# Kernel optimization log

Hardware: AMD Instinct MI355X
Metric: run time of the kernel (lower is better)

Reference implementation:

```python
import jax, jax.numpy as jnp
import numpy as np

N_NODES = 100000
N_EDGES = 1600000
MAX_RADIUS = 3.0
NUM_BASIS = 3
SQRT2 = 2.0 ** 0.5
# e3nn soft_one_hot_linspace 'smooth_finite' prefactor
C_SMOOTH = 1.14136 * float(np.exp(2.0))


def _sus(x):
    # smooth unit step: exp(-1/x) for x>0 else 0 (NaN-safe for grad)
    safe = jnp.where(x > 0.0, x, 1.0)
    return jnp.where(x > 0.0, jnp.exp(-1.0 / safe), 0.0)


def radial_embed(d):
    # soft_one_hot_linspace(d, 0, max_radius, 3, basis='smooth_finite', cutoff=True) * sqrt(num_basis)
    values = jnp.linspace(0.0, MAX_RADIUS, NUM_BASIS + 2)[1:-1]  # [3]
    step = MAX_RADIUS / (NUM_BASIS + 1)
    diff = (d[:, None] - values) / step  # [E,3]
    y = C_SMOOTH * _sus(diff + 1.0) * _sus(1.0 - diff)
    return y * (NUM_BASIS ** 0.5)


def fcnet(x, w1, w2):
    # e3nn FullyConnectedNet([3,16,numel], relu): normalized weights, normalize2mom(relu)=sqrt(2)*relu
    h = SQRT2 * jax.nn.relu(x @ (w1 / w1.shape[0] ** 0.5))
    return h @ (w2 / w2.shape[0] ** 0.5)


def reference(pos, feat, edge_src, edge_dst, fc1_w1, fc1_w2, core_w1, core_w2, fc3_w1, fc3_w2, conv_w, conv_b):
    n = pos.shape[0]
    z = edge_src.shape[0] / n  # average num neighbors
    edge_vec = pos[edge_dst] - pos[edge_src]
    d = jnp.sqrt(jnp.sum(edge_vec * edge_vec, axis=1))  # edges are self-loop-free -> d > 0
    emb = radial_embed(d)  # [E,3]

    # NOTE on e3nn math: with input/mid/output parities all even and sh = 0e+1o+2e,
    # the only parity-allowed paths producing nonzero output are the 0e (scalar) paths,
    # which contract against Y_0 = 1 ('component' normalization). The 4x1e block of the
    # mid irreps is identically zero (no parity-allowed path ever populates it), so the
    # math below (scalar block only, with e3nn path weights) is exactly equivalent.
    def conv(x, w1, w2, mul_in, mul_out, path_w):
        # per-edge weights from radial MLP; keep the 0e->0e instruction block
        w = fcnet(emb, w1, w2)[:, : mul_in * mul_out].reshape(-1, mul_in, mul_out)
        msg = path_w * jnp.einsum('euw,eu->ew', w, x[edge_src])
        return jax.ops.segment_sum(msg, edge_dst, num_segments=n) / z ** 0.5

    x = conv(feat, fc1_w1, fc1_w2, 3, 4, (1.0 / 3.0) ** 0.5)  # tp1: fan_in 3*1 -> pw=1/sqrt(3)
    for i in range(3):
        x = conv(x, core_w1[i], core_w2[i], 4, 4, 0.5)  # tp2 0e path: pw=sqrt(1/4)
    x = conv(x, fc3_w1, fc3_w2, 4, 16, 0.5)  # tp3: pw=sqrt(1/4)
    # Conv1d(16, 2, 1) == pointwise linear
    return x @ conv_w.T + conv_b


def setup_inputs():
    key = jax.random.key(0)
    ks = jax.random.split(key, 12)
    pos = jax.random.uniform(ks[0], (N_NODES, 3), dtype=jnp.float32)  # unit box -> all edge lengths < max_radius
    feat = jax.random.normal(ks[1], (N_NODES, 3), dtype=jnp.float32)
    edge_src = jax.random.randint(ks[2], (N_EDGES,), 0, N_NODES, dtype=jnp.int32)
    off = jax.random.randint(ks[3], (N_EDGES,), 1, N_NODES, dtype=jnp.int32)
    edge_dst = ((edge_src + off) % N_NODES).astype(jnp.int32)  # radius_graph has no self-loops
    return {
        'pos': pos,
        'feat': feat,
        'edge_src': edge_src,
        'edge_dst': edge_dst,
        'fc1_w1': jax.random.normal(ks[4], (3, 16), jnp.float32),
        'fc1_w2': jax.random.normal(ks[5], (16, 12), jnp.float32),
        'core_w1': jax.random.normal(ks[6], (3, 3, 16), jnp.float32),
        'core_w2': jax.random.normal(ks[7], (3, 16, 48), jnp.float32),
        'fc3_w1': jax.random.normal(ks[8], (3, 16), jnp.float32),
        'fc3_w2': jax.random.normal(ks[9], (16, 64), jnp.float32),
        'conv_w': jax.random.normal(ks[10], (2, 16), jnp.float32) * 0.25,
        'conv_b': jax.random.normal(ks[11], (2,), jnp.float32) * 0.1,
    }
```

## Files before the change

### kernel.cpp

```cpp
#include <hip/hip_runtime.h>


#define BCAP 4608
#define NBMAX 400

__device__ __forceinline__ float sus_f(float x) {
    return x > 0.0f ? __expf(-1.0f / x) : 0.0f;
}

__device__ __forceinline__ float uload(const float* p) {
    return __uint_as_float(__builtin_amdgcn_readfirstlane(__float_as_uint(*p)));
}

__global__ __launch_bounds__(256) void k_bin(
    const int* __restrict__ src, const int* __restrict__ dst,
    int* __restrict__ gcur, int* __restrict__ ptmp,
    const float* __restrict__ fc3w2, const float* __restrict__ cw,
    float* __restrict__ gbuf,
    int nedges, int nb)
{
    __shared__ int cnt[NBMAX];
    __shared__ int gb[NBMAX];
    for (int b = threadIdx.x; b < nb; b += 256) cnt[b] = 0;
    __syncthreads();

    int base = blockIdx.x * 2048 + threadIdx.x * 8;
    int pk[8]; int bk[8]; short r[8];
    int ss[8], dd[8];
    if (base + 7 < nedges) {
        int4 s0 = *(const int4*)&src[base];
        int4 s1 = *(const int4*)&src[base + 4];
        int4 d0 = *(const int4*)&dst[base];
        int4 d1 = *(const int4*)&dst[base + 4];
        ss[0]=s0.x; ss[1]=s0.y; ss[2]=s0.z; ss[3]=s0.w;
        ss[4]=s1.x; ss[5]=s1.y; ss[6]=s1.z; ss[7]=s1.w;
        dd[0]=d0.x; dd[1]=d0.y; dd[2]=d0.z; dd[3]=d0.w;
        dd[4]=d1.x; dd[5]=d1.y; dd[6]=d1.z; dd[7]=d1.w;
        #pragma unroll
        for (int i = 0; i < 8; ++i) {
            int b = dd[i] >> 8;
            bk[i] = b;
            pk[i] = (ss[i] << 8) | (dd[i] & 255);
            r[i] = (short)atomicAdd(&cnt[b], 1);
        }
    } else {
        #pragma unroll
        for (int i = 0; i < 8; ++i) {
            int e = base + i;
            if (e < nedges) {
                int s = src[e], t = dst[e];
                int b = t >> 8;
                bk[i] = b;
                pk[i] = (s << 8) | (t & 255);
                r[i] = (short)atomicAdd(&cnt[b], 1);
            } else bk[i] = -1;
        }
    }
    __syncthreads();
    for (int b = threadIdx.x; b < nb; b += 256) {
        int c = cnt[b];
        gb[b] = c > 0 ? atomicAdd(&gcur[b], c) : 0;
    }
    __syncthreads();
    #pragma unroll
    for (int i = 0; i < 8; ++i) {
        if (bk[i] >= 0) {
            int p = gb[bk[i]] + (int)r[i];
            if (p < BCAP)
                ptmp[bk[i] * BCAP + p] = pk[i];
        }
    }

    if (blockIdx.x == 0 && threadIdx.x < 128) {
        int idx = threadIdx.x;
        int k = idx >> 3, u = (idx >> 1) & 3, c = idx & 1;
        float s = 0.0f;
        #pragma unroll
        for (int w = 0; w < 16; ++w)
            s = fmaf(fc3w2[k * 64 + u * 16 + w], cw[c * 16 + w], s);
        gbuf[idx] = s;
    }
}

__global__ __launch_bounds__(256) void k_build(
    const int* __restrict__ gcur, const int* __restrict__ ptmp,
    int* __restrict__ pidx, int2* __restrict__ offs2,
    int n, int nb)
{
    int b = blockIdx.x;
    int cnt = gcur[b]; if (cnt > BCAP) cnt = BCAP;

    __shared__ int stage[BCAP];
    __shared__ int perm[BCAP];
    __shared__ int deg[256];
    __shared__ int loffs[256];
    __shared__ int cur[256];

    const int* tin = ptmp + b * BCAP;
    for (int j = threadIdx.x; j < cnt; j += 256) stage[j] = tin[j];
    deg[threadIdx.x] = 0;
    __syncthreads();

    for (int j = threadIdx.x; j < cnt; j += 256)
        atomicAdd(&deg[stage[j] & 255], 1);
    __syncthreads();

    {
        int t = threadIdx.x;
        int v = deg[t];
        loffs[t] = v; __syncthreads();
        for (int off = 1; off < 256; off <<= 1) {
            int val = (t >= off) ? loffs[t - off] : 0;
            __syncthreads();
            loffs[t] += val;
            __syncthreads();
        }
        int incl = loffs[t];
        __syncthreads();
        loffs[t] = incl - v;
        cur[t] = incl - v;
        __syncthreads();
    }

    {
        int nid0 = b << 8;
        int nn = n - nid0; if (nn > 256) nn = 256;
        int t = threadIdx.x;
        if (t < nn) {
            int st = b * BCAP + loffs[t];
            offs2[nid0 + t] = make_int2(st, st + deg[t]);
        }
    }

    for (int j = threadIdx.x; j < cnt; j += 256) {
        int pkd = stage[j];
        perm[atomicAdd(&cur[pkd & 255], 1)] = pkd;
    }
    __syncthreads();

    int* tout = pidx + b * BCAP;
    for (int j = threadIdx.x; j < cnt; j += 256) tout[j] = perm[j];
}

__global__ __launch_bounds__(256) void k_emb(
    const float* __restrict__ pos, const int* __restrict__ gcur,
    const int* __restrict__ pidx, float4* __restrict__ ebuf)
{
    int b = blockIdx.y;
    int j = blockIdx.x * 256 + threadIdx.x;
    if (j >= gcur[b]) return;
    int pkd = pidx[b * BCAP + j];
    int s = pkd >> 8;
    int t = (b << 8) | (pkd & 255);
    float dx = pos[3 * t + 0] - pos[3 * s + 0];
    float dy = pos[3 * t + 1] - pos[3 * s + 1];
    float dz = pos[3 * t + 2] - pos[3 * s + 2];
    float d = sqrtf(dx * dx + dy * dy + dz * dz);
    const float C = 1.14136f * 7.3890560989306495f;
    float e0, e1, e2;
    { float f = (d - 0.75f) * (1.0f / 0.75f);
      e0 = C * sus_f(f + 1.0f) * sus_f(1.0f - f); }
    { float f = (d - 1.50f) * (1.0f / 0.75f);
      e1 = C * sus_f(f + 1.0f) * sus_f(1.0f - f); }
    { float f = (d - 2.25f) * (1.0f / 0.75f);
      e2 = C * sus_f(f + 1.0f) * sus_f(1.0f - f); }
    ebuf[(size_t)b * BCAP + j] = make_float4(__int_as_float(s), e0, e1, e2);
}


__global__ __launch_bounds__(256) void k_node_l1(
    const float* __restrict__ feat, const float4* __restrict__ edata,
    const int2* __restrict__ offs2,
    const float* __restrict__ w1, const float* __restrict__ w2,
    float* __restrict__ xout, int n)
{
    __shared__ float lw[16 * 20];
    if (threadIdx.x < 192) {
        int k = threadIdx.x / 12, r = threadIdx.x % 12;
        lw[k * 20 + r] = w2[k * 12 + r];
    }
    __syncthreads();

    int g = blockIdx.x * 256 + threadIdx.x;
    int nd = g >> 2;
    if (nd >= n) return;
    int t = g & 3;

    float w1r[3][16];
    #pragma unroll
    for (int j = 0; j < 3; ++j)
        #pragma unroll
        for (int k = 0; k < 16; ++k) w1r[j][k] = uload(&w1[j * 16 + k]);

    float O[16][3];
    #pragma unroll
    for (int k = 0; k < 16; ++k)
        #pragma unroll
        for (int u = 0; u < 3; ++u) O[k][u] = 0.0f;

    int2 se = offs2[nd];
    for (int e = se.x + t; e < se.y; e += 4) {
        float4 ed = edata[e];
        int s = __float_as_int(ed.x);
        float f0 = feat[3 * s + 0], f1 = feat[3 * s + 1], f2 = feat[3 * s + 2];
        #pragma unroll
        for (int k = 0; k < 16; ++k) {
            float a = fmaf(ed.y, w1r[0][k], fmaf(ed.z, w1r[1][k], ed.w * w1r[2][k]));
            float h = a > 0.0f ? a : 0.0f;
            O[k][0] = fmaf(h, f0, O[k][0]);
            O[k][1] = fmaf(h, f1, O[k][1]);
            O[k][2] = fmaf(h, f2, O[k][2]);
        }
    }

    float p0 = 0.f, p1 = 0.f, p2 = 0.f, p3 = 0.f;
    #pragma unroll
    for (int k = 0; k < 16; ++k)
        #pragma unroll
        for (int u = 0; u < 3; ++u) {
            const float4 q = *(const float4*)&lw[k * 20 + u * 4];
            float o = O[k][u];
            p0 = fmaf(o, q.x, p0); p1 = fmaf(o, q.y, p1);
            p2 = fmaf(o, q.z, p2); p3 = fmaf(o, q.w, p3);
        }
    p0 += __shfl_xor(p0, 1); p1 += __shfl_xor(p1, 1);
    p2 += __shfl_xor(p2, 1); p3 += __shfl_xor(p3, 1);
    p0 += __shfl_xor(p0, 2); p1 += __shfl_xor(p1, 2);
    p2 += __shfl_xor(p2, 2); p3 += __shfl_xor(p3, 2);
    if (t == 0) {
        const float S = 0.051031036307982884f;
        float4 o; o.x = p0 * S; o.y = p1 * S; o.z = p2 * S; o.w = p3 * S;
        ((float4*)xout)[nd] = o;
    }
}

__global__ __launch_bounds__(256) void k_node_core(
    const float4* __restrict__ xin, const float4* __restrict__ edata,
    const int2* __restrict__ offs2,
    const float* __restrict__ w1, const float* __restrict__ w2,
    float* __restrict__ xout, int n)
{
    __shared__ float lw[16 * 20];
    {
        int idx = threadIdx.x;
        int k = idx >> 4, r = idx & 15;
        lw[k * 20 + r] = w2[k * 48 + r];
    }
    __syncthreads();

    int g = blockIdx.x * 256 + threadIdx.x;
    int nd = g >> 2;
    if (nd >= n) return;
    int t = g & 3;

    float w1r[3][16];
    #pragma unroll
    for (int j = 0; j < 3; ++j)
        #pragma unroll
        for (int k = 0; k < 16; ++k) w1r[j][k] = uload(&w1[j * 16 + k]);

    float O[16][4];
    #pragma unroll
    for (int k = 0; k < 16; ++k)
        #pragma unroll
        for (int u = 0; u < 4; ++u) O[k][u] = 0.0f;

    int2 se = offs2[nd];
    for (int e = se.x + t; e < se.y; e += 4) {
        float4 ed = edata[e];
        int s = __float_as_int(ed.x);
        float4 x = xin[s];
        #pragma unroll
        for (int k = 0; k < 16; ++k) {
            float a = fmaf(ed.y, w1r[0][k], fmaf(ed.z, w1r[1][k], ed.w * w1r[2][k]));
            float h = a > 0.0f ? a : 0.0f;
            O[k][0] = fmaf(h, x.x, O[k][0]);
            O[k][1] = fmaf(h, x.y, O[k][1]);
            O[k][2] = fmaf(h, x.z, O[k][2]);
            O[k][3] = fmaf(h, x.w, O[k][3]);
        }
    }

    float p0 = 0.f, p1 = 0.f, p2 = 0.f, p3 = 0.f;
    #pragma unroll
    for (int k = 0; k < 16; ++k)
        #pragma unroll
        for (int u = 0; u < 4; ++u) {
            const float4 q = *(const float4*)&lw[k * 20 + u * 4];
            float o = O[k][u];
            p0 = fmaf(o, q.x, p0); p1 = fmaf(o, q.y, p1);
            p2 = fmaf(o, q.z, p2); p3 = fmaf(o, q.w, p3);
        }
    p0 += __shfl_xor(p0, 1); p1 += __shfl_xor(p1, 1);
    p2 += __shfl_xor(p2, 1); p3 += __shfl_xor(p3, 1);
    p0 += __shfl_xor(p0, 2); p1 += __shfl_xor(p1, 2);
    p2 += __shfl_xor(p2, 2); p3 += __shfl_xor(p3, 2);
    if (t == 0) {
        const float S = 0.04419417382415922f;
        float4 o; o.x = p0 * S; o.y = p1 * S; o.z = p2 * S; o.w = p3 * S;
        ((float4*)xout)[nd] = o;
    }
}

__global__ __launch_bounds__(256) void k_node_fc3_final(
    const float4* __restrict__ xin, const float4* __restrict__ edata,
    const int2* __restrict__ offs2,
    const float* __restrict__ w1, const float* __restrict__ gbuf,
    const float* __restrict__ cb,
    float* __restrict__ out, int n)
{
    __shared__ float lg[128];
    if (threadIdx.x < 128) lg[threadIdx.x] = gbuf[threadIdx.x];
    __syncthreads();

    int g = blockIdx.x * 256 + threadIdx.x;
    int nd = g >> 2;
    if (nd >= n) return;
    int t = g & 3;

    float w1r[3][16];
    #pragma unroll
    for (int j = 0; j < 3; ++j)
        #pragma unroll
        for (int k = 0; k < 16; ++k) w1r[j][k] = uload(&w1[j * 16 + k]);

    float O[16][4];
    #pragma unroll
    for (int k = 0; k < 16; ++k)
        #pragma unroll
        for (int u = 0; u < 4; ++u) O[k][u] = 0.0f;

    int2 se = offs2[nd];
    for (int e = se.x + t; e < se.y; e += 4) {
        float4 ed = edata[e];
        int s = __float_as_int(ed.x);
        float4 x = xin[s];
        #pragma unroll
        for (int k = 0; k < 16; ++k) {
            float a = fmaf(ed.y, w1r[0][k], fmaf(ed.z, w1r[1][k], ed.w * w1r[2][k]));
            float h = a > 0.0f ? a : 0.0f;
            O[k][0] = fmaf(h, x.x, O[k][0]);
            O[k][1] = fmaf(h, x.y, O[k][1]);
            O[k][2] = fmaf(h, x.z, O[k][2]);
            O[k][3] = fmaf(h, x.w, O[k][3]);
        }
    }

    float a0 = 0.f, a1 = 0.f;
    #pragma unroll
    for (int k = 0; k < 16; ++k)
        #pragma unroll
        for (int u = 0; u < 4; ++u) {
            float o = O[k][u];
            const float2 q = *(const float2*)&lg[(k * 4 + u) * 2];
            a0 = fmaf(o, q.x, a0);
            a1 = fmaf(o, q.y, a1);
        }
    a0 += __shfl_xor(a0, 1); a1 += __shfl_xor(a1, 1);
    a0 += __shfl_xor(a0, 2); a1 += __shfl_xor(a1, 2);
    if (t == 0) {
        const float S = 0.04419417382415922f;
        float2 o; o.x = fmaf(a0, S, cb[0]); o.y = fmaf(a1, S, cb[1]);
        ((float2*)out)[nd] = o;
    }
}


extern "C" void kernel_launch(void* const* d_in, const int* in_sizes, int n_in,
                              void* d_out, int out_size, void* d_ws, size_t ws_size,
                              hipStream_t stream) {
    const float* pos     = (const float*)d_in[0];
    const float* feat    = (const float*)d_in[1];
    const int*   esrc    = (const int*)d_in[2];
    const int*   edst    = (const int*)d_in[3];
    const float* fc1_w1  = (const float*)d_in[4];
    const float* fc1_w2  = (const float*)d_in[5];
    const float* core_w1 = (const float*)d_in[6];
    const float* core_w2 = (const float*)d_in[7];
    const float* fc3_w1  = (const float*)d_in[8];
    const float* fc3_w2  = (const float*)d_in[9];
    const float* conv_w  = (const float*)d_in[10];
    const float* conv_b  = (const float*)d_in[11];
    float* out = (float*)d_out;

    const int E = in_sizes[2];
    const int N = in_sizes[0] / 3;
    const int nb = (N + 255) >> 8;

    float4* ebuf = (float4*)d_ws;
    int* ptmp  = (int*)(ebuf + (size_t)nb * BCAP);
    int* pidx  = ptmp + (size_t)nb * BCAP;
    float* xa  = (float*)(pidx + (size_t)nb * BCAP);
    float* xb  = xa + (size_t)4 * N;
    int2* offs2 = (int2*)(xb + (size_t)4 * N);
    int* gcur  = (int*)(offs2 + N);
    float* gbuf = (float*)(gcur + ((nb + 3) & ~3));

    int g4 = (4 * N + 255) / 256;

    hipMemsetAsync(gcur, 0, (size_t)nb * sizeof(int), stream);
    k_bin<<<(E + 2047) / 2048, 256, 0, stream>>>(esrc, edst, gcur, ptmp,
                                                 fc3_w2, conv_w, gbuf, E, nb);
    k_build<<<nb, 256, 0, stream>>>(gcur, ptmp, pidx, offs2, N, nb);
    {
        dim3 eg(BCAP / 256, nb);
        k_emb<<<eg, 256, 0, stream>>>(pos, gcur, pidx, ebuf);
    }

    k_node_l1<<<g4, 256, 0, stream>>>(feat, ebuf, offs2, fc1_w1, fc1_w2, xa, N);
    k_node_core<<<g4, 256, 0, stream>>>((const float4*)xa, ebuf, offs2,
                                        core_w1 + 0, core_w2 + 0, xb, N);
    k_node_core<<<g4, 256, 0, stream>>>((const float4*)xb, ebuf, offs2,
                                        core_w1 + 48, core_w2 + 768, xa, N);
    k_node_core<<<g4, 256, 0, stream>>>((const float4*)xa, ebuf, offs2,
                                        core_w1 + 96, core_w2 + 1536, xb, N);
    k_node_fc3_final<<<g4, 256, 0, stream>>>((const float4*)xb, ebuf, offs2,
                                             fc3_w1, gbuf, conv_b, out, N);
}
```

Measured before the change: 236.6 us.

## Fuse five node-layer kernels into one cooperative persistent kernel with grid syncs

Replaces the five per-layer node kernels with a single cooperative kernel. It loops over tiles persistently and places grid.sync between layers, sized from occupancy times 256 CUs. This removes four kernel launches and their tail and drain gaps. In exchange it adds grid-wide barrier costs, and __launch_bounds__(256,4) may cap registers or occupancy for the unrolled 64-accumulator loops.

```diff
diff --git a/kernel.cpp b/kernel.cpp
--- a/kernel.cpp
+++ b/kernel.cpp
@@ -1,4 +1,7 @@
 #include <hip/hip_runtime.h>
+#include <hip/hip_cooperative_groups.h>
+
+namespace cg = cooperative_groups;
 
 
 #define BCAP 4608
@@ -167,201 +170,206 @@
     ebuf[(size_t)b * BCAP + j] = make_float4(__int_as_float(s), e0, e1, e2);
 }
 
-
-__global__ __launch_bounds__(256) void k_node_l1(
+__global__ __launch_bounds__(256, 4) void k_layers(
     const float* __restrict__ feat, const float4* __restrict__ edata,
     const int2* __restrict__ offs2,
-    const float* __restrict__ w1, const float* __restrict__ w2,
-    float* __restrict__ xout, int n)
+    const float* __restrict__ fc1w1, const float* __restrict__ fc1w2,
+    const float* __restrict__ corew1, const float* __restrict__ corew2,
+    const float* __restrict__ fc3w1, const float* __restrict__ gbuf,
+    const float* __restrict__ cb,
+    float* __restrict__ xa, float* __restrict__ xb,
+    float* __restrict__ out, int n)
 {
     __shared__ float lw[16 * 20];
+    cg::grid_group grid = cg::this_grid();
+    const int items = 4 * n;
+    const int ntiles = (items + 255) >> 8;
+    const int t = threadIdx.x & 3;
+
     if (threadIdx.x < 192) {
         int k = threadIdx.x / 12, r = threadIdx.x % 12;
-        lw[k * 20 + r] = w2[k * 12 + r];
-    }
-    __syncthreads();
-
-    int g = blockIdx.x * 256 + threadIdx.x;
-    int nd = g >> 2;
-    if (nd >= n) return;
-    int t = g & 3;
-
-    float w1r[3][16];
-    #pragma unroll
-    for (int j = 0; j < 3; ++j)
-        #pragma unroll
-        for (int k = 0; k < 16; ++k) w1r[j][k] = uload(&w1[j * 16 + k]);
-
-    float O[16][3];
-    #pragma unroll
-    for (int k = 0; k < 16; ++k)
-        #pragma unroll
-        for (int u = 0; u < 3; ++u) O[k][u] = 0.0f;
-
-    int2 se = offs2[nd];
-    for (int e = se.x + t; e < se.y; e += 4) {
-        float4 ed = edata[e];
-        int s = __float_as_int(ed.x);
-        float f0 = feat[3 * s + 0], f1 = feat[3 * s + 1], f2 = feat[3 * s + 2];
-        #pragma unroll
-        for (int k = 0; k < 16; ++k) {
-            float a = fmaf(ed.y, w1r[0][k], fmaf(ed.z, w1r[1][k], ed.w * w1r[2][k]));
-            float h = a > 0.0f ? a : 0.0f;
-            O[k][0] = fmaf(h, f0, O[k][0]);
-            O[k][1] = fmaf(h, f1, O[k][1]);
-            O[k][2] = fmaf(h, f2, O[k][2]);
-        }
-    }
-
-    float p0 = 0.f, p1 = 0.f, p2 = 0.f, p3 = 0.f;
-    #pragma unroll
-    for (int k = 0; k < 16; ++k)
-        #pragma unroll
-        for (int u = 0; u < 3; ++u) {
-            const float4 q = *(const float4*)&lw[k * 20 + u * 4];
-            float o = O[k][u];
-            p0 = fmaf(o, q.x, p0); p1 = fmaf(o, q.y, p1);
-            p2 = fmaf(o, q.z, p2); p3 = fmaf(o, q.w, p3);
-        }
-    p0 += __shfl_xor(p0, 1); p1 += __shfl_xor(p1, 1);
-    p2 += __shfl_xor(p2, 1); p3 += __shfl_xor(p3, 1);
-    p0 += __shfl_xor(p0, 2); p1 += __shfl_xor(p1, 2);
-    p2 += __shfl_xor(p2, 2); p3 += __shfl_xor(p3, 2);
-    if (t == 0) {
-        const float S = 0.051031036307982884f;
-        float4 o; o.x = p0 * S; o.y = p1 * S; o.z = p2 * S; o.w = p3 * S;
-        ((float4*)xout)[nd] = o;
-    }
-}
-
-__global__ __launch_bounds__(256) void k_node_core(
-    const float4* __restrict__ xin, const float4* __restrict__ edata,
-    const int2* __restrict__ offs2,
-    const float* __restrict__ w1, const float* __restrict__ w2,
-    float* __restrict__ xout, int n)
-{
-    __shared__ float lw[16 * 20];
-    {
-        int idx = threadIdx.x;
-        int k = idx >> 4, r = idx & 15;
-        lw[k * 20 + r] = w2[k * 48 + r];
-    }
-    __syncthreads();
-
-    int g = blockIdx.x * 256 + threadIdx.x;
-    int nd = g >> 2;
-    if (nd >= n) return;
-    int t = g & 3;
-
-    float w1r[3][16];
-    #pragma unroll
-    for (int j = 0; j < 3; ++j)
-        #pragma unroll
-        for (int k = 0; k < 16; ++k) w1r[j][k] = uload(&w1[j * 16 + k]);
-
-    float O[16][4];
-    #pragma unroll
-    for (int k = 0; k < 16; ++k)
-        #pragma unroll
-        for (int u = 0; u < 4; ++u) O[k][u] = 0.0f;
-
-    int2 se = offs2[nd];
-    for (int e = se.x + t; e < se.y; e += 4) {
-        float4 ed = edata[e];
-        int s = __float_as_int(ed.x);
-        float4 x = xin[s];
-        #pragma unroll
-        for (int k = 0; k < 16; ++k) {
-            float a = fmaf(ed.y, w1r[0][k], fmaf(ed.z, w1r[1][k], ed.w * w1r[2][k]));
-            float h = a > 0.0f ? a : 0.0f;
-            O[k][0] = fmaf(h, x.x, O[k][0]);
-            O[k][1] = fmaf(h, x.y, O[k][1]);
-            O[k][2] = fmaf(h, x.z, O[k][2]);
-            O[k][3] = fmaf(h, x.w, O[k][3]);
-        }
-    }
-
-    float p0 = 0.f, p1 = 0.f, p2 = 0.f, p3 = 0.f;
-    #pragma unroll
-    for (int k = 0; k < 16; ++k)
-        #pragma unroll
-        for (int u = 0; u < 4; ++u) {
-            const float4 q = *(const float4*)&lw[k * 20 + u * 4];
-            float o = O[k][u];
-            p0 = fmaf(o, q.x, p0); p1 = fmaf(o, q.y, p1);
-            p2 = fmaf(o, q.z, p2); p3 = fmaf(o, q.w, p3);
-        }
-    p0 += __shfl_xor(p0, 1); p1 += __shfl_xor(p1, 1);
-    p2 += __shfl_xor(p2, 1); p3 += __shfl_xor(p3, 1);
-    p0 += __shfl_xor(p0, 2); p1 += __shfl_xor(p1, 2);
-    p2 += __shfl_xor(p2, 2); p3 += __shfl_xor(p3, 2);
-    if (t == 0) {
-        const float S = 0.04419417382415922f;
-        float4 o; o.x = p0 * S; o.y = p1 * S; o.z = p2 * S; o.w = p3 * S;
-        ((float4*)xout)[nd] = o;
-    }
-}
-
-__global__ __launch_bounds__(256) void k_node_fc3_final(
-    const float4* __restrict__ xin, const float4* __restrict__ edata,
-    const int2* __restrict__ offs2,
-    const float* __restrict__ w1, const float* __restrict__ gbuf,
-    const float* __restrict__ cb,
-    float* __restrict__ out, int n)
-{
-    __shared__ float lg[128];
-    if (threadIdx.x < 128) lg[threadIdx.x] = gbuf[threadIdx.x];
-    __syncthreads();
-
-    int g = blockIdx.x * 256 + threadIdx.x;
-    int nd = g >> 2;
-    if (nd >= n) return;
-    int t = g & 3;
-
-    float w1r[3][16];
-    #pragma unroll
-    for (int j = 0; j < 3; ++j)
-        #pragma unroll
-        for (int k = 0; k < 16; ++k) w1r[j][k] = uload(&w1[j * 16 + k]);
-
-    float O[16][4];
-    #pragma unroll
-    for (int k = 0; k < 16; ++k)
-        #pragma unroll
-        for (int u = 0; u < 4; ++u) O[k][u] = 0.0f;
-
-    int2 se = offs2[nd];
-    for (int e = se.x + t; e < se.y; e += 4) {
-        float4 ed = edata[e];
-        int s = __float_as_int(ed.x);
-        float4 x = xin[s];
-        #pragma unroll
-        for (int k = 0; k < 16; ++k) {
-            float a = fmaf(ed.y, w1r[0][k], fmaf(ed.z, w1r[1][k], ed.w * w1r[2][k]));
-            float h = a > 0.0f ? a : 0.0f;
-            O[k][0] = fmaf(h, x.x, O[k][0]);
-            O[k][1] = fmaf(h, x.y, O[k][1]);
-            O[k][2] = fmaf(h, x.z, O[k][2]);
-            O[k][3] = fmaf(h, x.w, O[k][3]);
-        }
-    }
-
-    float a0 = 0.f, a1 = 0.f;
-    #pragma unroll
-    for (int k = 0; k < 16; ++k)
-        #pragma unroll
-        for (int u = 0; u < 4; ++u) {
-            float o = O[k][u];
-            const float2 q = *(const float2*)&lg[(k * 4 + u) * 2];
-            a0 = fmaf(o, q.x, a0);
-            a1 = fmaf(o, q.y, a1);
-        }
-    a0 += __shfl_xor(a0, 1); a1 += __shfl_xor(a1, 1);
-    a0 += __shfl_xor(a0, 2); a1 += __shfl_xor(a1, 2);
-    if (t == 0) {
-        const float S = 0.04419417382415922f;
-        float2 o; o.x = fmaf(a0, S, cb[0]); o.y = fmaf(a1, S, cb[1]);
-        ((float2*)out)[nd] = o;
+        lw[k * 20 + r] = fc1w2[k * 12 + r];
+    }
+    __syncthreads();
+    {
+        float w1r[3][16];
+        #pragma unroll
+        for (int j = 0; j < 3; ++j)
+            #pragma unroll
+            for (int k = 0; k < 16; ++k) w1r[j][k] = uload(&fc1w1[j * 16 + k]);
+
+        for (int tile = blockIdx.x; tile < ntiles; tile += gridDim.x) {
+            int it = (tile << 8) + threadIdx.x;
+            if (it >= items) continue;
+            int nd = it >> 2;
+
+            float O[16][3];
+            #pragma unroll
+            for (int k = 0; k < 16; ++k)
+                #pragma unroll
+                for (int u = 0; u < 3; ++u) O[k][u] = 0.0f;
+
+            int2 se = offs2[nd];
+            for (int e = se.x + t; e < se.y; e += 4) {
+                float4 ed = edata[e];
+                int s = __float_as_int(ed.x);
+                float f0 = feat[3 * s + 0], f1 = feat[3 * s + 1], f2 = feat[3 * s + 2];
+                #pragma unroll
+                for (int k = 0; k < 16; ++k) {
+                    float a = fmaf(ed.y, w1r[0][k], fmaf(ed.z, w1r[1][k], ed.w * w1r[2][k]));
+                    float h = a > 0.0f ? a : 0.0f;
+                    O[k][0] = fmaf(h, f0, O[k][0]);
+                    O[k][1] = fmaf(h, f1, O[k][1]);
+                    O[k][2] = fmaf(h, f2, O[k][2]);
+                }
+            }
+
+            float p0 = 0.f, p1 = 0.f, p2 = 0.f, p3 = 0.f;
+            #pragma unroll
+            for (int k = 0; k < 16; ++k)
+                #pragma unroll
+                for (int u = 0; u < 3; ++u) {
+                    const float4 q = *(const float4*)&lw[k * 20 + u * 4];
+                    float o = O[k][u];
+                    p0 = fmaf(o, q.x, p0); p1 = fmaf(o, q.y, p1);
+                    p2 = fmaf(o, q.z, p2); p3 = fmaf(o, q.w, p3);
+                }
+            p0 += __shfl_xor(p0, 1); p1 += __shfl_xor(p1, 1);
+            p2 += __shfl_xor(p2, 1); p3 += __shfl_xor(p3, 1);
+            p0 += __shfl_xor(p0, 2); p1 += __shfl_xor(p1, 2);
+            p2 += __shfl_xor(p2, 2); p3 += __shfl_xor(p3, 2);
+            if (t == 0) {
+                const float S = 0.051031036307982884f;
+                float4 o; o.x = p0 * S; o.y = p1 * S; o.z = p2 * S; o.w = p3 * S;
+                ((float4*)xa)[nd] = o;
+            }
+        }
+    }
+    grid.sync();
+
+    for (int c = 0; c < 3; ++c) {
+        const float*  w1p  = corew1 + 48 * c;
+        const float*  w2p  = corew2 + 768 * c;
+        const float4* xin  = (const float4*)((c == 1) ? xb : xa);
+        float*        xout = (c == 1) ? xa : xb;
+
+        {
+            int k = threadIdx.x >> 4, r = threadIdx.x & 15;
+            lw[k * 20 + r] = w2p[k * 48 + r];
+        }
+        __syncthreads();
+
+        float w1r[3][16];
+        #pragma unroll
+        for (int j = 0; j < 3; ++j)
+            #pragma unroll
+            for (int k = 0; k < 16; ++k) w1r[j][k] = uload(&w1p[j * 16 + k]);
+
+        for (int tile = blockIdx.x; tile < ntiles; tile += gridDim.x) {
+            int it = (tile << 8) + threadIdx.x;
+            if (it >= items) continue;
+            int nd = it >> 2;
+
+            float O[16][4];
+            #pragma unroll
+            for (int k = 0; k < 16; ++k)
+                #pragma unroll
+                for (int u = 0; u < 4; ++u) O[k][u] = 0.0f;
+
+            int2 se = offs2[nd];
+            for (int e = se.x + t; e < se.y; e += 4) {
+                float4 ed = edata[e];
+                int s = __float_as_int(ed.x);
+                float4 x = xin[s];
+                #pragma unroll
+                for (int k = 0; k < 16; ++k) {
+                    float a = fmaf(ed.y, w1r[0][k], fmaf(ed.z, w1r[1][k], ed.w * w1r[2][k]));
+                    float h = a > 0.0f ? a : 0.0f;
+                    O[k][0] = fmaf(h, x.x, O[k][0]);
+                    O[k][1] = fmaf(h, x.y, O[k][1]);
+                    O[k][2] = fmaf(h, x.z, O[k][2]);
+                    O[k][3] = fmaf(h, x.w, O[k][3]);
+                }
+            }
+
+            float p0 = 0.f, p1 = 0.f, p2 = 0.f, p3 = 0.f;
+            #pragma unroll
+            for (int k = 0; k < 16; ++k)
+                #pragma unroll
+                for (int u = 0; u < 4; ++u) {
+                    const float4 q = *(const float4*)&lw[k * 20 + u * 4];
+                    float o = O[k][u];
+                    p0 = fmaf(o, q.x, p0); p1 = fmaf(o, q.y, p1);
+                    p2 = fmaf(o, q.z, p2); p3 = fmaf(o, q.w, p3);
+                }
+            p0 += __shfl_xor(p0, 1); p1 += __shfl_xor(p1, 1);
+            p2 += __shfl_xor(p2, 1); p3 += __shfl_xor(p3, 1);
+            p0 += __shfl_xor(p0, 2); p1 += __shfl_xor(p1, 2);
+            p2 += __shfl_xor(p2, 2); p3 += __shfl_xor(p3, 2);
+            if (t == 0) {
+                const float S = 0.04419417382415922f;
+                float4 o; o.x = p0 * S; o.y = p1 * S; o.z = p2 * S; o.w = p3 * S;
+                ((float4*)xout)[nd] = o;
+            }
+        }
+        grid.sync();
+    }
+
+    if (threadIdx.x < 128) lw[threadIdx.x] = gbuf[threadIdx.x];
+    __syncthreads();
+    {
+        const float4* xin = (const float4*)xb;
+        float w1r[3][16];
+        #pragma unroll
+        for (int j = 0; j < 3; ++j)
+            #pragma unroll
+            for (int k = 0; k < 16; ++k) w1r[j][k] = uload(&fc3w1[j * 16 + k]);
+
+        for (int tile = blockIdx.x; tile < ntiles; tile += gridDim.x) {
+            int it = (tile << 8) + threadIdx.x;
+            if (it >= items) continue;
+            int nd = it >> 2;
+
+            float O[16][4];
+            #pragma unroll
+            for (int k = 0; k < 16; ++k)
+                #pragma unroll
+                for (int u = 0; u < 4; ++u) O[k][u] = 0.0f;
+
+            int2 se = offs2[nd];
+            for (int e = se.x + t; e < se.y; e += 4) {
+                float4 ed = edata[e];
+                int s = __float_as_int(ed.x);
+                float4 x = xin[s];
+                #pragma unroll
+                for (int k = 0; k < 16; ++k) {
+                    float a = fmaf(ed.y, w1r[0][k], fmaf(ed.z, w1r[1][k], ed.w * w1r[2][k]));
+                    float h = a > 0.0f ? a : 0.0f;
+                    O[k][0] = fmaf(h, x.x, O[k][0]);
+                    O[k][1] = fmaf(h, x.y, O[k][1]);
+                    O[k][2] = fmaf(h, x.z, O[k][2]);
+                    O[k][3] = fmaf(h, x.w, O[k][3]);
+                }
+            }
+
+            float a0 = 0.f, a1 = 0.f;
+            #pragma unroll
+            for (int k = 0; k < 16; ++k)
+                #pragma unroll
+                for (int u = 0; u < 4; ++u) {
+                    float o = O[k][u];
+                    const float2 q = *(const float2*)&lw[(k * 4 + u) * 2];
+                    a0 = fmaf(o, q.x, a0);
+                    a1 = fmaf(o, q.y, a1);
+                }
+            a0 += __shfl_xor(a0, 1); a1 += __shfl_xor(a1, 1);
+            a0 += __shfl_xor(a0, 2); a1 += __shfl_xor(a1, 2);
+            if (t == 0) {
+                const float S = 0.04419417382415922f;
+                float2 o; o.x = fmaf(a0, S, cb[0]); o.y = fmaf(a1, S, cb[1]);
+                ((float2*)out)[nd] = o;
+            }
+        }
     }
 }
 
@@ -396,8 +404,6 @@
     int* gcur  = (int*)(offs2 + N);
     float* gbuf = (float*)(gcur + ((nb + 3) & ~3));
 
-    int g4 = (4 * N + 255) / 256;
-
     hipMemsetAsync(gcur, 0, (size_t)nb * sizeof(int), stream);
     k_bin<<<(E + 2047) / 2048, 256, 0, stream>>>(esrc, edst, gcur, ptmp,
                                                  fc3_w2, conv_w, gbuf, E, nb);
@@ -407,13 +413,23 @@
         k_emb<<<eg, 256, 0, stream>>>(pos, gcur, pidx, ebuf);
     }
 
-    k_node_l1<<<g4, 256, 0, stream>>>(feat, ebuf, offs2, fc1_w1, fc1_w2, xa, N);
-    k_node_core<<<g4, 256, 0, stream>>>((const float4*)xa, ebuf, offs2,
-                                        core_w1 + 0, core_w2 + 0, xb, N);
-    k_node_core<<<g4, 256, 0, stream>>>((const float4*)xb, ebuf, offs2,
-                                        core_w1 + 48, core_w2 + 768, xa, N);
-    k_node_core<<<g4, 256, 0, stream>>>((const float4*)xa, ebuf, offs2,
-                                        core_w1 + 96, core_w2 + 1536, xb, N);
-    k_node_fc3_final<<<g4, 256, 0, stream>>>((const float4*)xb, ebuf, offs2,
-                                             fc3_w1, gbuf, conv_b, out, N);
-}
+    {
+        int nbpc = 0;
+        hipOccupancyMaxActiveBlocksPerMultiprocessor(
+            &nbpc, reinterpret_cast<const void*>(k_layers), 256, 0);
+        if (nbpc < 1) nbpc = 1;
+        int ntiles = (4 * N + 255) / 256;
+        int gsize = nbpc * 256;
+        if (gsize > ntiles) gsize = ntiles;
+
+        void* kargs[] = {
+            (void*)&feat, (void*)&ebuf, (void*)&offs2,
+            (void*)&fc1_w1, (void*)&fc1_w2,
+            (void*)&core_w1, (void*)&core_w2,
+            (void*)&fc3_w1, (void*)&gbuf, (void*)&conv_b,
+            (void*)&xa, (void*)&xb, (void*)&out, (void*)&N
+        };
+        hipLaunchCooperativeKernel(reinterpret_cast<const void*>(k_layers),
+                                   dim3(gsize), dim3(256), kargs, 0, stream);
+    }
+}
```

Result: slower. 859.0 us (+263.0%).

## Balance edge work per block with contiguous chunks and LDS atomic accumulation

Applied to the files above, without the earlier changes.

Replaces the four-threads-per-node split with a scheme where each 128-node block divides its contiguous CSR edge range evenly across 256 threads. Each thread accumulates the partial 16x4 hidden-feature sums for runs of edges that share a destination node, then flushes them into a per-node shared-memory accumulator with LDS atomics. The per-node output projection is done afterwards from shared memory. The goal is to remove load imbalance caused by varying node degrees. The cost is LDS atomics at run boundaries, a large shared-memory footprint that limits occupancy, and the edge buffer now storing the packed index so each thread can find the destination.

```diff
diff --git a/kernel.cpp b/kernel.cpp
--- a/kernel.cpp
+++ b/kernel.cpp
@@ -3,6 +3,7 @@
 
 #define BCAP 4608
 #define NBMAX 400
+#define OSTR 68
 
 __device__ __forceinline__ float sus_f(float x) {
     return x > 0.0f ? __expf(-1.0f / x) : 0.0f;
@@ -164,27 +165,34 @@
       e1 = C * sus_f(f + 1.0f) * sus_f(1.0f - f); }
     { float f = (d - 2.25f) * (1.0f / 0.75f);
       e2 = C * sus_f(f + 1.0f) * sus_f(1.0f - f); }
-    ebuf[(size_t)b * BCAP + j] = make_float4(__int_as_float(s), e0, e1, e2);
-}
-
-
-__global__ __launch_bounds__(256) void k_node_l1(
+    ebuf[(size_t)b * BCAP + j] = make_float4(__int_as_float(pkd), e0, e1, e2);
+}
+
+
+__global__ __launch_bounds__(256) void k_layer_l1(
     const float* __restrict__ feat, const float4* __restrict__ edata,
     const int2* __restrict__ offs2,
     const float* __restrict__ w1, const float* __restrict__ w2,
     float* __restrict__ xout, int n)
 {
+    __shared__ float Oacc[128 * OSTR];
     __shared__ float lw[16 * 20];
     if (threadIdx.x < 192) {
         int k = threadIdx.x / 12, r = threadIdx.x % 12;
         lw[k * 20 + r] = w2[k * 12 + r];
     }
-    __syncthreads();
-
-    int g = blockIdx.x * 256 + threadIdx.x;
-    int nd = g >> 2;
-    if (nd >= n) return;
-    int t = g & 3;
+    for (int i = threadIdx.x; i < 128 * OSTR; i += 256) Oacc[i] = 0.0f;
+    __syncthreads();
+
+    int base = blockIdx.x * 128;
+    int nn = n - base; if (nn > 128) nn = 128;
+    int e0 = offs2[base].x;
+    int e1 = offs2[base + nn - 1].y;
+    int cnt = e1 - e0;
+    int chunk = (cnt + 255) >> 8;
+    int js = e0 + threadIdx.x * chunk;
+    int je = js + chunk; if (je > e1) je = e1;
+    int lnbase = base & 255;
 
     float w1r[3][16];
     #pragma unroll
@@ -193,15 +201,25 @@
         for (int k = 0; k < 16; ++k) w1r[j][k] = uload(&w1[j * 16 + k]);
 
     float O[16][3];
-    #pragma unroll
-    for (int k = 0; k < 16; ++k)
-        #pragma unroll
-        for (int u = 0; u < 3; ++u) O[k][u] = 0.0f;
-
-    int2 se = offs2[nd];
-    for (int e = se.x + t; e < se.y; e += 4) {
-        float4 ed = edata[e];
-        int s = __float_as_int(ed.x);
+    int cur = -1;
+    for (int j = js; j < je; ++j) {
+        float4 ed = edata[j];
+        int pkd = __float_as_int(ed.x);
+        int ln = (pkd & 255) - lnbase;
+        int s = pkd >> 8;
+        if (ln != cur) {
+            if (cur >= 0) {
+                #pragma unroll
+                for (int k = 0; k < 16; ++k) {
+                    atomicAdd(&Oacc[cur * OSTR + k * 4 + 0], O[k][0]);
+                    atomicAdd(&Oacc[cur * OSTR + k * 4 + 1], O[k][1]);
+                    atomicAdd(&Oacc[cur * OSTR + k * 4 + 2], O[k][2]);
+                }
+            }
+            cur = ln;
+            #pragma unroll
+            for (int k = 0; k < 16; ++k) { O[k][0] = 0.f; O[k][1] = 0.f; O[k][2] = 0.f; }
+        }
         float f0 = feat[3 * s + 0], f1 = feat[3 * s + 1], f2 = feat[3 * s + 2];
         #pragma unroll
         for (int k = 0; k < 16; ++k) {
@@ -212,46 +230,60 @@
             O[k][2] = fmaf(h, f2, O[k][2]);
         }
     }
-
-    float p0 = 0.f, p1 = 0.f, p2 = 0.f, p3 = 0.f;
-    #pragma unroll
-    for (int k = 0; k < 16; ++k)
-        #pragma unroll
-        for (int u = 0; u < 3; ++u) {
-            const float4 q = *(const float4*)&lw[k * 20 + u * 4];
-            float o = O[k][u];
-            p0 = fmaf(o, q.x, p0); p1 = fmaf(o, q.y, p1);
-            p2 = fmaf(o, q.z, p2); p3 = fmaf(o, q.w, p3);
-        }
-    p0 += __shfl_xor(p0, 1); p1 += __shfl_xor(p1, 1);
-    p2 += __shfl_xor(p2, 1); p3 += __shfl_xor(p3, 1);
-    p0 += __shfl_xor(p0, 2); p1 += __shfl_xor(p1, 2);
-    p2 += __shfl_xor(p2, 2); p3 += __shfl_xor(p3, 2);
-    if (t == 0) {
+    if (cur >= 0) {
+        #pragma unroll
+        for (int k = 0; k < 16; ++k) {
+            atomicAdd(&Oacc[cur * OSTR + k * 4 + 0], O[k][0]);
+            atomicAdd(&Oacc[cur * OSTR + k * 4 + 1], O[k][1]);
+            atomicAdd(&Oacc[cur * OSTR + k * 4 + 2], O[k][2]);
+        }
+    }
+    __syncthreads();
+
+    int t = threadIdx.x;
+    if (t < nn) {
+        float p0 = 0.f, p1 = 0.f, p2 = 0.f, p3 = 0.f;
+        #pragma unroll
+        for (int k = 0; k < 16; ++k) {
+            float4 o = *(const float4*)&Oacc[t * OSTR + k * 4];
+            const float4 q0 = *(const float4*)&lw[k * 20 + 0];
+            const float4 q1 = *(const float4*)&lw[k * 20 + 4];
+            const float4 q2 = *(const float4*)&lw[k * 20 + 8];
+            p0 = fmaf(o.x, q0.x, fmaf(o.y, q1.x, fmaf(o.z, q2.x, p0)));
+            p1 = fmaf(o.x, q0.y, fmaf(o.y, q1.y, fmaf(o.z, q2.y, p1)));
+            p2 = fmaf(o.x, q0.z, fmaf(o.y, q1.z, fmaf(o.z, q2.z, p2)));
+            p3 = fmaf(o.x, q0.w, fmaf(o.y, q1.w, fmaf(o.z, q2.w, p3)));
+        }
         const float S = 0.051031036307982884f;
         float4 o; o.x = p0 * S; o.y = p1 * S; o.z = p2 * S; o.w = p3 * S;
-        ((float4*)xout)[nd] = o;
-    }
-}
-
-__global__ __launch_bounds__(256) void k_node_core(
+        ((float4*)xout)[base + t] = o;
+    }
+}
+
+__global__ __launch_bounds__(256) void k_layer_core(
     const float4* __restrict__ xin, const float4* __restrict__ edata,
     const int2* __restrict__ offs2,
     const float* __restrict__ w1, const float* __restrict__ w2,
     float* __restrict__ xout, int n)
 {
+    __shared__ float Oacc[128 * OSTR];
     __shared__ float lw[16 * 20];
     {
-        int idx = threadIdx.x;
-        int k = idx >> 4, r = idx & 15;
+        int k = threadIdx.x >> 4, r = threadIdx.x & 15;
         lw[k * 20 + r] = w2[k * 48 + r];
     }
-    __syncthreads();
-
-    int g = blockIdx.x * 256 + threadIdx.x;
-    int nd = g >> 2;
-    if (nd >= n) return;
-    int t = g & 3;
+    for (int i = threadIdx.x; i < 128 * OSTR; i += 256) Oacc[i] = 0.0f;
+    __syncthreads();
+
+    int base = blockIdx.x * 128;
+    int nn = n - base; if (nn > 128) nn = 128;
+    int e0 = offs2[base].x;
+    int e1 = offs2[base + nn - 1].y;
+    int cnt = e1 - e0;
+    int chunk = (cnt + 255) >> 8;
+    int js = e0 + threadIdx.x * chunk;
+    int je = js + chunk; if (je > e1) je = e1;
+    int lnbase = base & 255;
 
     float w1r[3][16];
     #pragma unroll
@@ -260,15 +292,28 @@
         for (int k = 0; k < 16; ++k) w1r[j][k] = uload(&w1[j * 16 + k]);
 
     float O[16][4];
-    #pragma unroll
-    for (int k = 0; k < 16; ++k)
-        #pragma unroll
-        for (int u = 0; u < 4; ++u) O[k][u] = 0.0f;
-
-    int2 se = offs2[nd];
-    for (int e = se.x + t; e < se.y; e += 4) {
-        float4 ed = edata[e];
-        int s = __float_as_int(ed.x);
+    int cur = -1;
+    for (int j = js; j < je; ++j) {
+        float4 ed = edata[j];
+        int pkd = __float_as_int(ed.x);
+        int ln = (pkd & 255) - lnbase;
+        int s = pkd >> 8;
+        if (ln != cur) {
+            if (cur >= 0) {
+                #pragma unroll
+                for (int k = 0; k < 16; ++k) {
+                    atomicAdd(&Oacc[cur * OSTR + k * 4 + 0], O[k][0]);
+                    atomicAdd(&Oacc[cur * OSTR + k * 4 + 1], O[k][1]);
+                    atomicAdd(&Oacc[cur * OSTR + k * 4 + 2], O[k][2]);
+                    atomicAdd(&Oacc[cur * OSTR + k * 4 + 3], O[k][3]);
+                }
+            }
+            cur = ln;
+            #pragma unroll
+            for (int k = 0; k < 16; ++k) {
+                O[k][0] = 0.f; O[k][1] = 0.f; O[k][2] = 0.f; O[k][3] = 0.f;
+            }
+        }
         float4 x = xin[s];
         #pragma unroll
         for (int k = 0; k < 16; ++k) {
@@ -280,43 +325,60 @@
             O[k][3] = fmaf(h, x.w, O[k][3]);
         }
     }
-
-    float p0 = 0.f, p1 = 0.f, p2 = 0.f, p3 = 0.f;
-    #pragma unroll
-    for (int k = 0; k < 16; ++k)
-        #pragma unroll
-        for (int u = 0; u < 4; ++u) {
-            const float4 q = *(const float4*)&lw[k * 20 + u * 4];
-            float o = O[k][u];
-            p0 = fmaf(o, q.x, p0); p1 = fmaf(o, q.y, p1);
-            p2 = fmaf(o, q.z, p2); p3 = fmaf(o, q.w, p3);
-        }
-    p0 += __shfl_xor(p0, 1); p1 += __shfl_xor(p1, 1);
-    p2 += __shfl_xor(p2, 1); p3 += __shfl_xor(p3, 1);
-    p0 += __shfl_xor(p0, 2); p1 += __shfl_xor(p1, 2);
-    p2 += __shfl_xor(p2, 2); p3 += __shfl_xor(p3, 2);
-    if (t == 0) {
+    if (cur >= 0) {
+        #pragma unroll
+        for (int k = 0; k < 16; ++k) {
+            atomicAdd(&Oacc[cur * OSTR + k * 4 + 0], O[k][0]);
+            atomicAdd(&Oacc[cur * OSTR + k * 4 + 1], O[k][1]);
+            atomicAdd(&Oacc[cur * OSTR + k * 4 + 2], O[k][2]);
+            atomicAdd(&Oacc[cur * OSTR + k * 4 + 3], O[k][3]);
+        }
+    }
+    __syncthreads();
+
+    int t = threadIdx.x;
+    if (t < nn) {
+        float p0 = 0.f, p1 = 0.f, p2 = 0.f, p3 = 0.f;
+        #pragma unroll
+        for (int k = 0; k < 16; ++k) {
+            float4 o = *(const float4*)&Oacc[t * OSTR + k * 4];
+            const float4 q0 = *(const float4*)&lw[k * 20 + 0];
+            const float4 q1 = *(const float4*)&lw[k * 20 + 4];
+            const float4 q2 = *(const float4*)&lw[k * 20 + 8];
+            const float4 q3 = *(const float4*)&lw[k * 20 + 12];
+            p0 = fmaf(o.x, q0.x, fmaf(o.y, q1.x, fmaf(o.z, q2.x, fmaf(o.w, q3.x, p0))));
+            p1 = fmaf(o.x, q0.y, fmaf(o.y, q1.y, fmaf(o.z, q2.y, fmaf(o.w, q3.y, p1))));
+            p2 = fmaf(o.x, q0.z, fmaf(o.y, q1.z, fmaf(o.z, q2.z, fmaf(o.w, q3.z, p2))));
+            p3 = fmaf(o.x, q0.w, fmaf(o.y, q1.w, fmaf(o.z, q2.w, fmaf(o.w, q3.w, p3))));
+        }
         const float S = 0.04419417382415922f;
         float4 o; o.x = p0 * S; o.y = p1 * S; o.z = p2 * S; o.w = p3 * S;
-        ((float4*)xout)[nd] = o;
-    }
-}
-
-__global__ __launch_bounds__(256) void k_node_fc3_final(
+        ((float4*)xout)[base + t] = o;
+    }
+}
+
+__global__ __launch_bounds__(256) void k_layer_fc3(
     const float4* __restrict__ xin, const float4* __restrict__ edata,
     const int2* __restrict__ offs2,
     const float* __restrict__ w1, const float* __restrict__ gbuf,
     const float* __restrict__ cb,
     float* __restrict__ out, int n)
 {
+    __shared__ float Oacc[128 * OSTR];
     __shared__ float lg[128];
     if (threadIdx.x < 128) lg[threadIdx.x] = gbuf[threadIdx.x];
-    __syncthreads();
-
-    int g = blockIdx.x * 256 + threadIdx.x;
-    int nd = g >> 2;
-    if (nd >= n) return;
-    int t = g & 3;
+    for (int i = threadIdx.x; i < 128 * OSTR; i += 256) Oacc[i] = 0.0f;
+    __syncthreads();
+
+    int base = blockIdx.x * 128;
+    int nn = n - base; if (nn > 128) nn = 128;
+    int e0 = offs2[base].x;
+    int e1 = offs2[base + nn - 1].y;
+    int cnt = e1 - e0;
+    int chunk = (cnt + 255) >> 8;
+    int js = e0 + threadIdx.x * chunk;
+    int je = js + chunk; if (je > e1) je = e1;
+    int lnbase = base & 255;
 
     float w1r[3][16];
     #pragma unroll
@@ -325,15 +387,28 @@
         for (int k = 0; k < 16; ++k) w1r[j][k] = uload(&w1[j * 16 + k]);
 
     float O[16][4];
-    #pragma unroll
-    for (int k = 0; k < 16; ++k)
-        #pragma unroll
-        for (int u = 0; u < 4; ++u) O[k][u] = 0.0f;
-
-    int2 se = offs2[nd];
-    for (int e = se.x + t; e < se.y; e += 4) {
-        float4 ed = edata[e];
-        int s = __float_as_int(ed.x);
+    int cur = -1;
+    for (int j = js; j < je; ++j) {
+        float4 ed = edata[j];
+        int pkd = __float_as_int(ed.x);
+        int ln = (pkd & 255) - lnbase;
+        int s = pkd >> 8;
+        if (ln != cur) {
+            if (cur >= 0) {
+                #pragma unroll
+                for (int k = 0; k < 16; ++k) {
+                    atomicAdd(&Oacc[cur * OSTR + k * 4 + 0], O[k][0]);
+                    atomicAdd(&Oacc[cur * OSTR + k * 4 + 1], O[k][1]);
+                    atomicAdd(&Oacc[cur * OSTR + k * 4 + 2], O[k][2]);
+                    atomicAdd(&Oacc[cur * OSTR + k * 4 + 3], O[k][3]);
+                }
+            }
+            cur = ln;
+            #pragma unroll
+            for (int k = 0; k < 16; ++k) {
+                O[k][0] = 0.f; O[k][1] = 0.f; O[k][2] = 0.f; O[k][3] = 0.f;
+            }
+        }
         float4 x = xin[s];
         #pragma unroll
         for (int k = 0; k < 16; ++k) {
@@ -345,23 +420,31 @@
             O[k][3] = fmaf(h, x.w, O[k][3]);
         }
     }
-
-    float a0 = 0.f, a1 = 0.f;
-    #pragma unroll
-    for (int k = 0; k < 16; ++k)
-        #pragma unroll
-        for (int u = 0; u < 4; ++u) {
-            float o = O[k][u];
-            const float2 q = *(const float2*)&lg[(k * 4 + u) * 2];
-            a0 = fmaf(o, q.x, a0);
-            a1 = fmaf(o, q.y, a1);
-        }
-    a0 += __shfl_xor(a0, 1); a1 += __shfl_xor(a1, 1);
-    a0 += __shfl_xor(a0, 2); a1 += __shfl_xor(a1, 2);
-    if (t == 0) {
+    if (cur >= 0) {
+        #pragma unroll
+        for (int k = 0; k < 16; ++k) {
+            atomicAdd(&Oacc[cur * OSTR + k * 4 + 0], O[k][0]);
+            atomicAdd(&Oacc[cur * OSTR + k * 4 + 1], O[k][1]);
+            atomicAdd(&Oacc[cur * OSTR + k * 4 + 2], O[k][2]);
+            atomicAdd(&Oacc[cur * OSTR + k * 4 + 3], O[k][3]);
+        }
+    }
+    __syncthreads();
+
+    int t = threadIdx.x;
+    if (t < nn) {
+        float a0 = 0.f, a1 = 0.f;
+        #pragma unroll
+        for (int k = 0; k < 16; ++k) {
+            float4 o = *(const float4*)&Oacc[t * OSTR + k * 4];
+            const float4 g0 = *(const float4*)&lg[k * 8 + 0];
+            const float4 g1 = *(const float4*)&lg[k * 8 + 4];
+            a0 = fmaf(o.x, g0.x, fmaf(o.y, g0.z, fmaf(o.z, g1.x, fmaf(o.w, g1.z, a0))));
+            a1 = fmaf(o.x, g0.y, fmaf(o.y, g0.w, fmaf(o.z, g1.y, fmaf(o.w, g1.w, a1))));
+        }
         const float S = 0.04419417382415922f;
         float2 o; o.x = fmaf(a0, S, cb[0]); o.y = fmaf(a1, S, cb[1]);
-        ((float2*)out)[nd] = o;
+        ((float2*)out)[base + t] = o;
     }
 }
 
@@ -396,7 +479,7 @@
     int* gcur  = (int*)(offs2 + N);
     float* gbuf = (float*)(gcur + ((nb + 3) & ~3));
 
-    int g4 = (4 * N + 255) / 256;
+    int nblk = (N + 127) / 128;
 
     hipMemsetAsync(gcur, 0, (size_t)nb * sizeof(int), stream);
     k_bin<<<(E + 2047) / 2048, 256, 0, stream>>>(esrc, edst, gcur, ptmp,
@@ -407,13 +490,14 @@
         k_emb<<<eg, 256, 0, stream>>>(pos, gcur, pidx, ebuf);
     }
 
-    k_node_l1<<<g4, 256, 0, stream>>>(feat, ebuf, offs2, fc1_w1, fc1_w2, xa, N);
-    k_node_core<<<g4, 256, 0, stream>>>((const float4*)xa, ebuf, offs2,
-                                        core_w1 + 0, core_w2 + 0, xb, N);
-    k_node_core<<<g4, 256, 0, stream>>>((const float4*)xb, ebuf, offs2,
-                                        core_w1 + 48, core_w2 + 768, xa, N);
-    k_node_core<<<g4, 256, 0, stream>>>((const float4*)xa, ebuf, offs2,
-                                        core_w1 + 96, core_w2 + 1536, xb, N);
-    k_node_fc3_final<<<g4, 256, 0, stream>>>((const float4*)xb, ebuf, offs2,
-                                             fc3_w1, gbuf, conv_b, out, N);
-}
+    k_layer_l1<<<nblk, 256, 0, stream>>>(feat, ebuf, offs2,
+                                         fc1_w1, fc1_w2, xa, N);
+    k_layer_core<<<nblk, 256, 0, stream>>>((const float4*)xa, ebuf, offs2,
+                                           core_w1 + 0, core_w2 + 0, xb, N);
+    k_layer_core<<<nblk, 256, 0, stream>>>((const float4*)xb, ebuf, offs2,
+                                           core_w1 + 48, core_w2 + 768, xa, N);
+    k_layer_core<<<nblk, 256, 0, stream>>>((const float4*)xa, ebuf, offs2,
+                                           core_w1 + 96, core_w2 + 1536, xb, N);
+    k_layer_fc3<<<nblk, 256, 0, stream>>>((const float4*)xb, ebuf, offs2,
+                                          fc3_w1, gbuf, conv_b, out, N);
+}
```

Measured after the change: 807.9 us. 3.41x slower.
